# Optimization experiments

Hardware: AMD Instinct MI355X
Metric: run time of the kernel (lower is better)

Reference implementation:

```python
import jax, jax.numpy as jnp
from jax import lax
import numpy as np

B, L, E, H, PRED = 2048, 107, 128, 128, 68
NG, NL, D3 = 3, 3, 384  # 3 stacked GRUs, 3 layers each, padded input dim 3*H


def setup_inputs() -> dict:
    key = jax.random.key(0)
    ks = jax.random.split(key, 10)
    s = 0.08  # ~1/sqrt(H), matches torch GRU init scale
    return {
        "encoded_sequence": jax.random.randint(ks[0], (B, L), 0, 14),
        "encoded_structure": jax.random.randint(ks[1], (B, L), 0, 14),
        "encoded_predicted_loop_type": jax.random.randint(ks[2], (B, L), 0, 14),
        "embed_table": jax.random.normal(ks[3], (14, E), jnp.float32) * s,
        "w_ih": jax.random.normal(ks[4], (NG, NL, 2, 3 * H, D3), jnp.float32) * s,
        "w_hh": jax.random.normal(ks[5], (NG, NL, 2, 3 * H, H), jnp.float32) * s,
        "b_ih": jax.random.normal(ks[6], (NG, NL, 2, 3 * H), jnp.float32) * s,
        "b_hh": jax.random.normal(ks[7], (NG, NL, 2, 3 * H), jnp.float32) * s,
        "lin_w": jax.random.normal(ks[8], (2 * H, 3), jnp.float32) * s,
        "lin_b": jax.random.normal(ks[9], (3,), jnp.float32) * s,
    }


def _gru_dir(x, Wih, Whh, bih, bhh, reverse):
    # x: [B, L, D3]; Wih: [3H, D3]; Whh: [3H, H]. PyTorch gate order: r, z, n.
    xp = jnp.einsum('bld,gd->blg', x, Wih) + bih  # precompute input projections [B,L,3H]
    if reverse:
        xp = xp[:, ::-1]

    def step(h, xt):
        gh = h @ Whh.T + bhh  # [B, 3H]
        xr, xz, xn = jnp.split(xt, 3, axis=-1)
        hr, hz, hn = jnp.split(gh, 3, axis=-1)
        r = jax.nn.sigmoid(xr + hr)
        z = jax.nn.sigmoid(xz + hz)
        n = jnp.tanh(xn + r * hn)
        hnew = (1.0 - z) * n + z * h
        return hnew, hnew

    h0 = jnp.zeros((x.shape[0], H), x.dtype)
    _, hs = lax.scan(step, h0, jnp.swapaxes(xp, 0, 1))  # [L, B, H]
    hs = jnp.swapaxes(hs, 0, 1)
    return hs[:, ::-1] if reverse else hs


def _pad_feat(x):
    d = x.shape[-1]
    return x if d == D3 else jnp.pad(x, ((0, 0), (0, 0), (0, D3 - d)))


def reference(encoded_sequence, encoded_structure, encoded_predicted_loop_type,
              embed_table, w_ih, w_hh, b_ih, b_hh, lin_w, lin_b):
    tok = jnp.stack([encoded_sequence, encoded_structure,
                     encoded_predicted_loop_type], axis=-1)  # [B, L, 3]
    out = embed_table[tok].reshape(tok.shape[0], L, 3 * E)  # [B, L, 384]
    for g in range(NG):
        for l in range(NL):
            xin = _pad_feat(out)
            f = _gru_dir(xin, w_ih[g, l, 0], w_hh[g, l, 0], b_ih[g, l, 0], b_hh[g, l, 0], False)
            b = _gru_dir(xin, w_ih[g, l, 1], w_hh[g, l, 1], b_ih[g, l, 1], b_hh[g, l, 1], True)
            out = jnp.concatenate([f, b], axis=-1)  # [B, L, 2H]
    return out[:, :PRED] @ lin_w + lin_b  # [B, pred_len, 3]
```

## Files before the change

### kernel.cpp

```cpp
#include <hip/hip_runtime.h>
#include <hip/hip_bf16.h>

#define B_ 2048
#define L_ 107
#define E_ 128
#define H_ 128
#define PRED_ 68
#define M_ (B_*L_)

typedef __bf16 bf16;
typedef __bf16 bf16x8 __attribute__((ext_vector_type(8)));
typedef __bf16 bf16x4 __attribute__((ext_vector_type(4)));
typedef float f32x4 __attribute__((ext_vector_type(4)));

__device__ __forceinline__ void gload16(const void* g, void* l) {
  __builtin_amdgcn_global_load_lds(
      (const __attribute__((address_space(1))) unsigned int*)g,
      (__attribute__((address_space(3))) unsigned int*)l, 16, 0, 0);
}

__device__ __forceinline__ float sigm(float x)  { return 1.f / (1.f + __expf(-x)); }
__device__ __forceinline__ float tanhx(float x) { return 1.f - 2.f / (1.f + __expf(2.f * x)); }

__global__ void pack_wih_k(const float* __restrict__ w_ih, bf16* __restrict__ out) {
  int idx = blockIdx.x * 256 + threadIdx.x;
  if (idx >= 9*12*6*8*64*8) return;
  int e = idx & 7;
  int lane = (idx >> 3) & 63;
  int q = idx >> 9;
  int nt = q & 7; q >>= 3;
  int nb = q % 6; q /= 6;
  int kt = q % 12; int gl = q / 12;
  int ng = nb*128 + nt*16 + (lane & 15);
  int k  = kt*32 + (lane >> 4)*8 + e;
  int d  = (ng >= 384) ? 1 : 0;
  int np = ng - d*384;
  float v = w_ih[(((size_t)(gl*2 + d)*384 + np)*384 + k)];
  out[idx] = (bf16)v;
}

__global__ void pack_whh_k(const float* __restrict__ w_hh, bf16* __restrict__ out) {
  int idx = blockIdx.x * 256 + threadIdx.x;
  if (idx >= 9*2*4*24*64*8) return;
  int e = idx & 7;
  int lane = (idx >> 3) & 63;
  int q = idx >> 9;
  int nt = q % 24; q /= 24;
  int ks = q & 3;  q >>= 2;
  int d  = q & 1;  int gl = q >> 1;
  int n = nt*16 + (lane & 15);
  int k = ks*32 + (lane >> 4)*8 + e;
  out[idx] = (bf16)w_hh[((size_t)(gl*2 + d)*384 + n)*128 + k];
}

__global__ void pack_bias_k(const float* __restrict__ b_ih, const float* __restrict__ b_hh,
                            float* __restrict__ bias, float* __restrict__ bhhn) {
  int idx = blockIdx.x * 256 + threadIdx.x;
  if (idx < 9*768) {
    int gl = idx / 768; int n = idx % 768;
    int d = (n >= 384) ? 1 : 0; int np = n - d*384;
    float v = b_ih[(gl*2 + d)*384 + np];
    if (np < 256) v += b_hh[(gl*2 + d)*384 + np];
    bias[idx] = v;
  }
  if (idx < 9*256) {
    int gl = idx / 256; int r = idx % 256;
    int d = (r >= 128) ? 1 : 0; int j = r & 127;
    bhhn[idx] = b_hh[(gl*2 + d)*384 + 256 + j];
  }
}

__global__ void shadow_k(const bf16* __restrict__ X, bf16* __restrict__ shlo,
                         bf16* __restrict__ shhi) {
  int idx = blockIdx.x * 256 + threadIdx.x;
  const int NLO = 2048*54*16;
  if (idx < NLO) {
    int k8 = idx & 15; int q = idx >> 4; int t = q % 54; int b = q / 54;
    *reinterpret_cast<bf16x8*>(shlo + ((size_t)b*54 + t)*128 + k8*8) =
      *reinterpret_cast<const bf16x8*>(X + ((size_t)b*107 + t)*256 + k8*8);
  } else {
    idx -= NLO;
    int k8 = idx & 15; int q = idx >> 4; int t = 54 + q % 53; int b = q / 53;
    if (b < 2048)
      *reinterpret_cast<bf16x8*>(shhi + ((size_t)b*53 + (t-54))*128 + k8*8) =
        *reinterpret_cast<const bf16x8*>(X + ((size_t)b*107 + t)*256 + 128 + k8*8);
  }
}

__global__ __launch_bounds__(256) void gemm_proj_k(
    const bf16* __restrict__ Xin, const bf16* __restrict__ shlo, const bf16* __restrict__ shhi,
    const int* __restrict__ seq, const int* __restrict__ str, const int* __restrict__ lp,
    const float* __restrict__ table, int L0, int KT,
    const bf16* __restrict__ Bp, const float* __restrict__ bias,
    bf16* __restrict__ xpw, int len, int t0f, int t0b) {
  __shared__ __align__(16) bf16 As[2][128*32];
  __shared__ __align__(16) bf16 Bs[2][512*8];
  __shared__ __align__(16) bf16 TBl[14*136];
  __shared__ int tokl[3*128];
  int tid = threadIdx.x; int lane = tid & 63; int w = tid >> 6;
  int l4 = lane & 15, g4 = lane >> 4;
  int wm = w >> 1, wn = w & 1;
  int tw = blockIdx.x >> 4, mtile = blockIdx.x & 15;
  int nb = blockIdx.y, d = blockIdx.z;
  int t = d ? (t0b - tw) : (t0f + tw);

  int c0 = tid, c1 = tid + 256;
  int r0 = c0 >> 2, cc0 = c0 & 3;
  int r1 = c1 >> 2, cc1 = c1 & 3;
  int sw0 = ((cc0 ^ ((r0 >> 1) & 3)) * 8), sw1 = ((cc1 ^ ((r1 >> 1) & 3)) * 8);
  int b0g = mtile*128 + r0, b1g = mtile*128 + r1;
  const bf16* xr0 = Xin + ((size_t)b0g*107 + t)*256;
  const bf16* xr1 = Xin + ((size_t)b1g*107 + t)*256;
  const bf16 *pLo0, *pHi0, *pLo1, *pHi1;
  if (d == 0) {
    pLo0 = xr0; pHi0 = (t < 54) ? xr0 : (shhi + ((size_t)b0g*53 + (t-54))*128 - 128);
    pLo1 = xr1; pHi1 = (t < 54) ? xr1 : (shhi + ((size_t)b1g*53 + (t-54))*128 - 128);
  } else {
    pHi0 = xr0; pLo0 = (t < 54) ? (shlo + ((size_t)b0g*54 + t)*128) : xr0;
    pHi1 = xr1; pLo1 = (t < 54) ? (shlo + ((size_t)b1g*54 + t)*128) : xr1;
  }
  const bf16* Bb = Bp + (size_t)(d*3 + nb) * 4096;

  if (L0) {
    for (int i = tid; i < 1792; i += 256) TBl[(i >> 7)*136 + (i & 127)] = (bf16)table[i];
    if (tid < 128) {
      int b = mtile*128 + tid;
      int g = b*107 + t;
      tokl[tid] = seq[g]; tokl[128 + tid] = str[g]; tokl[256 + tid] = lp[g];
    }
  }

  float bias_r[4];
  #pragma unroll
  for (int nt = 0; nt < 4; ++nt)
    bias_r[nt] = bias[d*384 + nb*128 + wn*64 + nt*16 + l4];

  f32x4 acc[4][4];
  #pragma unroll
  for (int i = 0; i < 4; ++i)
    #pragma unroll
    for (int j = 0; j < 4; ++j) { f32x4 z = {0.f,0.f,0.f,0.f}; acc[i][j] = z; }

  if (!L0) {
    gload16(pLo0 + sw0, &As[0][c0*8]);
    gload16(pLo1 + sw1, &As[0][c1*8]);
  }
  gload16(Bb + c0*8, &Bs[0][c0*8]);
  gload16(Bb + c1*8, &Bs[0][c1*8]);
  __syncthreads();

  for (int kt = 0; kt < KT; ++kt) {
    int cur = kt & 1, nxt = cur ^ 1;
    if (kt + 1 < KT) {
      int k1 = kt + 1;
      if (!L0) {
        gload16((k1 < 4 ? pLo0 : pHi0) + (size_t)k1*32 + sw0, &As[nxt][c0*8]);
        gload16((k1 < 4 ? pLo1 : pHi1) + (size_t)k1*32 + sw1, &As[nxt][c1*8]);
      }
      gload16(Bb + (size_t)k1*6*4096 + c0*8, &Bs[nxt][c0*8]);
      gload16(Bb + (size_t)k1*6*4096 + c1*8, &Bs[nxt][c1*8]);
    }
    bf16x8 af[4], bfr[4];
    if (L0) {
      int ch = kt >> 2; int kc = (kt & 3) * 32;
      #pragma unroll
      for (int mt = 0; mt < 4; ++mt) {
        int r = wm*64 + mt*16 + l4;
        af[mt] = *reinterpret_cast<const bf16x8*>(TBl + tokl[ch*128 + r]*136 + kc + g4*8);
      }
    } else {
      #pragma unroll
      for (int mt = 0; mt < 4; ++mt) {
        int r = wm*64 + mt*16 + l4;
        af[mt] = *reinterpret_cast<const bf16x8*>(&As[cur][r*32 + ((g4 ^ ((r >> 1) & 3)) * 8)]);
      }
    }
    #pragma unroll
    for (int nt = 0; nt < 4; ++nt)
      bfr[nt] = *reinterpret_cast<const bf16x8*>(&Bs[cur][((wn*4 + nt)*64 + lane)*8]);
    #pragma unroll
    for (int mt = 0; mt < 4; ++mt)
      #pragma unroll
      for (int nt = 0; nt < 4; ++nt)
        acc[mt][nt] = __builtin_amdgcn_mfma_f32_16x16x32_bf16(af[mt], bfr[nt], acc[mt][nt], 0, 0, 0);
    __syncthreads();
  }

  int tile_m_base = tw*128 + mtile*8 + wm*4;
  int tile_n_base = nb*8 + wn*4;
  size_t dbase = d ? (size_t)len*128*24*256 : 0;
  #pragma unroll
  for (int mt = 0; mt < 4; ++mt)
    #pragma unroll
    for (int nt = 0; nt < 4; ++nt) {
      f32x4 a = acc[mt][nt]; float bv = bias_r[nt];
      bf16x4 o;
      o[0] = (bf16)(a[0] + bv); o[1] = (bf16)(a[1] + bv);
      o[2] = (bf16)(a[2] + bv); o[3] = (bf16)(a[3] + bv);
      *reinterpret_cast<bf16x4*>(xpw + dbase +
          (((size_t)(tile_m_base + mt)*24 + tile_n_base + nt) << 8) + lane*4) = o;
    }
}

__global__ __launch_bounds__(512, 1) void scan_k(const bf16* __restrict__ xpw,
                                                 const bf16* __restrict__ whh,
                                                 const float* __restrict__ bhhn,
                                                 bf16* __restrict__ xout,
                                                 float* __restrict__ hst,
                                                 int len, int t0f, int t0b, int first) {
  __shared__ __align__(16) bf16 h_lds[2][2048];
  int tid = threadIdx.x; int lane = tid & 63; int w = tid >> 6;
  int l4 = lane & 15, g4 = lane >> 4;
  int d = blockIdx.y;
  int bx = blockIdx.x;
  int b0 = bx * 16;
  const bf16* xpb = xpw + (d ? (size_t)len*128*24*256 : 0);
  int ntl[3] = { w, 8 + w, 16 + w };
  int fragoff = g4*64 + l4*4;
  int j = w*16 + l4;
  int js = j >> 5, jc3 = (j >> 3) & 3, je = j & 7;

  bf16x8 bw[3][4];
  #pragma unroll
  for (int nt = 0; nt < 3; ++nt)
    #pragma unroll
    for (int ks = 0; ks < 4; ++ks)
      bw[nt][ks] = *reinterpret_cast<const bf16x8*>(whh + ((size_t)(d*4 + ks)*24 + ntl[nt])*512 + lane*8);

  float bn = bhhn[d*128 + j];
  float h_own[4];

  if (first) {
    #pragma unroll
    for (int i = 0; i < 4; ++i) h_own[i] = 0.f;
    if (tid < 256) reinterpret_cast<float4*>(&h_lds[0][0])[tid] = make_float4(0.f, 0.f, 0.f, 0.f);
  } else {
    #pragma unroll
    for (int i = 0; i < 4; ++i) {
      h_own[i] = hst[((size_t)d*2048 + b0 + g4*4 + i)*128 + j];
      int m = g4*4 + i;
      h_lds[0][(js*64 + m + 16*jc3)*8 + je] = (bf16)h_own[i];
    }
  }

  bf16x4 xa[3], xb[3];
  {
    #pragma unroll
    for (int nt = 0; nt < 3; ++nt)
      xa[nt] = *reinterpret_cast<const bf16x4*>(xpb + (((size_t)bx*24 + ntl[nt]) << 8) + fragoff);
  }
  __syncthreads();

  auto step = [&](bf16x4 (&xu)[3], bf16x4 (&xl)[3], int tw, int pb) {
    int tc = d ? (t0b - tw) : (t0f + tw);
    int twn = (tw + 1 < len) ? (tw + 1) : (len - 1);
    bf16x8 a[4];
    #pragma unroll
    for (int ks = 0; ks < 4; ++ks)
      a[ks] = *reinterpret_cast<const bf16x8*>(&h_lds[pb][(ks*64 + lane)*8]);
    size_t tmn = (size_t)(twn*128 + bx)*24;
    #pragma unroll
    for (int nt = 0; nt < 3; ++nt)
      xl[nt] = *reinterpret_cast<const bf16x4*>(xpb + ((tmn + ntl[nt]) << 8) + fragoff);
    f32x4 acc[3];
    #pragma unroll
    for (int nt = 0; nt < 3; ++nt) { f32x4 z = {0.f,0.f,0.f,0.f}; acc[nt] = z; }
    #pragma unroll
    for (int ks = 0; ks < 4; ++ks)
      #pragma unroll
      for (int nt = 0; nt < 3; ++nt)
        acc[nt] = __builtin_amdgcn_mfma_f32_16x16x32_bf16(a[ks], bw[nt][ks], acc[nt], 0, 0, 0);
    #pragma unroll
    for (int i = 0; i < 4; ++i) {
      float r = sigm((float)xu[0][i] + acc[0][i]);
      float z = sigm((float)xu[1][i] + acc[1][i]);
      float n = tanhx((float)xu[2][i] + r * (acc[2][i] + bn));
      float hv = (1.f - z) * n + z * h_own[i];
      h_own[i] = hv;
      int m = g4*4 + i;
      h_lds[pb ^ 1][(js*64 + m + 16*jc3)*8 + je] = (bf16)hv;
    }
    __syncthreads();
    if (tid < 256) {
      int mo = tid & 15, sc = tid >> 4;
      int s = sc >> 2, c3 = sc & 3;
      bf16x8 v = *reinterpret_cast<const bf16x8*>(&h_lds[pb ^ 1][s*512 + c3*128 + mo*8]);
      *reinterpret_cast<bf16x8*>(xout + ((size_t)(b0 + mo)*107 + tc)*256 + d*128 + s*32 + c3*8) = v;
    }
  };

  for (int tw = 0; tw < len; ++tw) {
    if (tw & 1) step(xb, xa, tw, 1);
    else        step(xa, xb, tw, 0);
  }
  #pragma unroll
  for (int i = 0; i < 4; ++i)
    hst[((size_t)d*2048 + b0 + g4*4 + i)*128 + j] = h_own[i];
}

__global__ void final_k(const bf16* __restrict__ hs, const float* __restrict__ lw,
                        const float* __restrict__ lb, float* __restrict__ out) {
  __shared__ float wsm[768];
  int tid = threadIdx.x;
  for (int i = tid; i < 768; i += 256) wsm[i] = lw[i];
  __syncthreads();
  int idx = blockIdx.x * 256 + tid;
  int b = idx / 68, t = idx % 68;
  const bf16* row = hs + (size_t)(b*107 + t) * 256;
  float a0 = lb[0], a1 = lb[1], a2 = lb[2];
  for (int j0 = 0; j0 < 256; j0 += 8) {
    bf16x8 v = *reinterpret_cast<const bf16x8*>(row + j0);
    #pragma unroll
    for (int e = 0; e < 8; ++e) {
      float f = (float)v[e];
      a0 += f * wsm[(j0 + e)*3 + 0];
      a1 += f * wsm[(j0 + e)*3 + 1];
      a2 += f * wsm[(j0 + e)*3 + 2];
    }
  }
  out[(size_t)idx*3 + 0] = a0;
  out[(size_t)idx*3 + 1] = a1;
  out[(size_t)idx*3 + 2] = a2;
}

extern "C" void kernel_launch(void* const* d_in, const int* in_sizes, int n_in,
                              void* d_out, int out_size, void* d_ws, size_t ws_size,
                              hipStream_t stream) {
  const int*   seq   = (const int*)d_in[0];
  const int*   str   = (const int*)d_in[1];
  const int*   lp    = (const int*)d_in[2];
  const float* table = (const float*)d_in[3];
  const float* w_ih  = (const float*)d_in[4];
  const float* w_hh  = (const float*)d_in[5];
  const float* b_ih  = (const float*)d_in[6];
  const float* b_hh  = (const float*)d_in[7];
  const float* lw    = (const float*)d_in[8];
  const float* lb    = (const float*)d_in[9];
  float* out = (float*)d_out;
  char* ws = (char*)d_ws;

  const size_t xsz    = (size_t)M_ * 256 * 2;
  const size_t shlosz = (size_t)2048*54*128*2;
  const size_t shhisz = (size_t)2048*53*128*2;
  const size_t wihsz  = (size_t)9*12*6*8*64*8 * 2;
  const size_t whhsz  = (size_t)9*2*4*24*64*8 * 2;
  const size_t biassz = 9*768*4, bhhnsz = 9*256*4;
  const size_t hstsz  = (size_t)2*2048*128*4;
  const size_t fixed  = xsz + shlosz + shhisz + wihsz + whhsz + biassz + bhhnsz + hstsz;
  int W = 32;
  while (W > 8 && fixed + (size_t)2*2048*W*384*2 > ws_size) W -= 8;
  const size_t xpwsz = (size_t)2*2048*W*384*2;

  size_t off = 0;
  bf16* X    = (bf16*)(ws + off); off += xsz;
  bf16* XPW  = (bf16*)(ws + off); off += xpwsz;
  bf16* SHLO = (bf16*)(ws + off); off += shlosz;
  bf16* SHHI = (bf16*)(ws + off); off += shhisz;
  bf16* WIH  = (bf16*)(ws + off); off += wihsz;
  bf16* WHH  = (bf16*)(ws + off); off += whhsz;
  float* BIAS = (float*)(ws + off); off += biassz;
  float* BHHN = (float*)(ws + off); off += bhhnsz;
  float* HST  = (float*)(ws + off);

  hipLaunchKernelGGL(pack_wih_k,  dim3(2654208/256), dim3(256), 0, stream, w_ih, WIH);
  hipLaunchKernelGGL(pack_whh_k,  dim3(884736/256),  dim3(256), 0, stream, w_hh, WHH);
  hipLaunchKernelGGL(pack_bias_k, dim3(27),          dim3(256), 0, stream, b_ih, b_hh, BIAS, BHHN);

  const int phases = (107 + W - 1) / W;
  for (int gl = 0; gl < 9; ++gl) {
    int L0 = (gl == 0) ? 1 : 0;
    int KT = L0 ? 12 : 8;
    if (!L0)
      hipLaunchKernelGGL(shadow_k, dim3(13696), dim3(256), 0, stream, X, SHLO, SHHI);
    for (int p = 0; p < phases; ++p) {
      int len = (107 - p*W < W) ? (107 - p*W) : W;
      int t0f = p*W;
      int t0b = 106 - p*W;
      hipLaunchKernelGGL(gemm_proj_k, dim3(len*16, 3, 2), dim3(256), 0, stream,
                         X, SHLO, SHHI, seq, str, lp, table, L0, KT,
                         WIH + (size_t)gl*294912, BIAS + gl*768, XPW, len, t0f, t0b);
      hipLaunchKernelGGL(scan_k, dim3(128, 2), dim3(512), 0, stream,
                         XPW, WHH + (size_t)gl*98304, BHHN + gl*256, X, HST,
                         len, t0f, t0b, (p == 0) ? 1 : 0);
    }
  }
  hipLaunchKernelGGL(final_k, dim3(544), dim3(256), 0, stream, X, lw, lb, out);
}
```

Before: 3.146 ms.

## Enlarge projection GEMM tile to 256 rows and use explicit vmcnt waits

The input-projection GEMM now covers 256 batch rows per block, with each wave computing a 64x128 output tile, so B-fragment loads are reused across twice as many rows and the grid is halved. The kernel is templated on the embedding-layer flag so the unused paths and shared buffers drop out at compile time. Full __syncthreads are replaced by raw s_barrier plus explicit s_waitcnt vmcnt counts, which lets the next tile's loads stay in flight during the current MFMA work. The cost is a larger accumulator array per thread (more registers, possibly lower occupancy) and fewer blocks per launch.

```diff
diff --git a/kernel.cpp b/kernel.cpp
--- a/kernel.cpp
+++ b/kernel.cpp
@@ -87,112 +87,122 @@
   }
 }
 
+template<int L0>
 __global__ __launch_bounds__(256) void gemm_proj_k(
     const bf16* __restrict__ Xin, const bf16* __restrict__ shlo, const bf16* __restrict__ shhi,
     const int* __restrict__ seq, const int* __restrict__ str, const int* __restrict__ lp,
-    const float* __restrict__ table, int L0, int KT,
+    const float* __restrict__ table, int KT,
     const bf16* __restrict__ Bp, const float* __restrict__ bias,
     bf16* __restrict__ xpw, int len, int t0f, int t0b) {
-  __shared__ __align__(16) bf16 As[2][128*32];
-  __shared__ __align__(16) bf16 Bs[2][512*8];
-  __shared__ __align__(16) bf16 TBl[14*136];
-  __shared__ int tokl[3*128];
+  __shared__ __align__(16) bf16 As[2][256*32];
+  __shared__ __align__(16) bf16 Bs[2][128*32];
+  __shared__ __align__(16) bf16 TBl[L0 ? 14*136 : 1];
+  __shared__ int tokl[L0 ? 3*256 : 1];
   int tid = threadIdx.x; int lane = tid & 63; int w = tid >> 6;
   int l4 = lane & 15, g4 = lane >> 4;
-  int wm = w >> 1, wn = w & 1;
-  int tw = blockIdx.x >> 4, mtile = blockIdx.x & 15;
+  int tw = blockIdx.x >> 3, mtile = blockIdx.x & 7;
   int nb = blockIdx.y, d = blockIdx.z;
   int t = d ? (t0b - tw) : (t0f + tw);
 
+  int rr[4], sw[4];
+  const bf16* pLo[4]; const bf16* pHi[4];
+  #pragma unroll
+  for (int i = 0; i < 4; ++i) {
+    int c = tid + 256*i;
+    int r = c >> 2, cc = c & 3;
+    rr[i] = r; sw[i] = (cc ^ ((r >> 1) & 3)) * 8;
+    int bg = mtile*256 + r;
+    const bf16* xr = Xin + ((size_t)bg*107 + t)*256;
+    if (d == 0) {
+      pLo[i] = xr; pHi[i] = (t < 54) ? xr : (shhi + ((size_t)bg*53 + (t-54))*128 - 128);
+    } else {
+      pHi[i] = xr; pLo[i] = (t < 54) ? (shlo + ((size_t)bg*54 + t)*128) : xr;
+    }
+  }
   int c0 = tid, c1 = tid + 256;
-  int r0 = c0 >> 2, cc0 = c0 & 3;
-  int r1 = c1 >> 2, cc1 = c1 & 3;
-  int sw0 = ((cc0 ^ ((r0 >> 1) & 3)) * 8), sw1 = ((cc1 ^ ((r1 >> 1) & 3)) * 8);
-  int b0g = mtile*128 + r0, b1g = mtile*128 + r1;
-  const bf16* xr0 = Xin + ((size_t)b0g*107 + t)*256;
-  const bf16* xr1 = Xin + ((size_t)b1g*107 + t)*256;
-  const bf16 *pLo0, *pHi0, *pLo1, *pHi1;
-  if (d == 0) {
-    pLo0 = xr0; pHi0 = (t < 54) ? xr0 : (shhi + ((size_t)b0g*53 + (t-54))*128 - 128);
-    pLo1 = xr1; pHi1 = (t < 54) ? xr1 : (shhi + ((size_t)b1g*53 + (t-54))*128 - 128);
-  } else {
-    pHi0 = xr0; pLo0 = (t < 54) ? (shlo + ((size_t)b0g*54 + t)*128) : xr0;
-    pHi1 = xr1; pLo1 = (t < 54) ? (shlo + ((size_t)b1g*54 + t)*128) : xr1;
-  }
   const bf16* Bb = Bp + (size_t)(d*3 + nb) * 4096;
 
-  if (L0) {
+  if constexpr (L0) {
     for (int i = tid; i < 1792; i += 256) TBl[(i >> 7)*136 + (i & 127)] = (bf16)table[i];
-    if (tid < 128) {
-      int b = mtile*128 + tid;
-      int g = b*107 + t;
-      tokl[tid] = seq[g]; tokl[128 + tid] = str[g]; tokl[256 + tid] = lp[g];
-    }
-  }
-
-  float bias_r[4];
-  #pragma unroll
-  for (int nt = 0; nt < 4; ++nt)
-    bias_r[nt] = bias[d*384 + nb*128 + wn*64 + nt*16 + l4];
-
-  f32x4 acc[4][4];
+    for (int i = tid; i < 768; i += 256) {
+      int b = mtile*256 + (i & 255);
+      const int* tokp = (i < 256) ? seq : ((i < 512) ? str : lp);
+      tokl[i] = tokp[b*107 + t];
+    }
+  }
+
+  float bias_r[8];
+  #pragma unroll
+  for (int nt = 0; nt < 8; ++nt)
+    bias_r[nt] = bias[d*384 + nb*128 + nt*16 + l4];
+
+  f32x4 acc[4][8];
   #pragma unroll
   for (int i = 0; i < 4; ++i)
     #pragma unroll
-    for (int j = 0; j < 4; ++j) { f32x4 z = {0.f,0.f,0.f,0.f}; acc[i][j] = z; }
-
-  if (!L0) {
-    gload16(pLo0 + sw0, &As[0][c0*8]);
-    gload16(pLo1 + sw1, &As[0][c1*8]);
+    for (int j = 0; j < 8; ++j) { f32x4 z = {0.f,0.f,0.f,0.f}; acc[i][j] = z; }
+
+  if constexpr (!L0) {
+    #pragma unroll
+    for (int i = 0; i < 4; ++i)
+      gload16(pLo[i] + sw[i], &As[0][(tid + 256*i)*8]);
   }
   gload16(Bb + c0*8, &Bs[0][c0*8]);
   gload16(Bb + c1*8, &Bs[0][c1*8]);
-  __syncthreads();
+  if constexpr (L0) __builtin_amdgcn_s_barrier();
 
   for (int kt = 0; kt < KT; ++kt) {
     int cur = kt & 1, nxt = cur ^ 1;
     if (kt + 1 < KT) {
       int k1 = kt + 1;
-      if (!L0) {
-        gload16((k1 < 4 ? pLo0 : pHi0) + (size_t)k1*32 + sw0, &As[nxt][c0*8]);
-        gload16((k1 < 4 ? pLo1 : pHi1) + (size_t)k1*32 + sw1, &As[nxt][c1*8]);
+      if constexpr (!L0) {
+        #pragma unroll
+        for (int i = 0; i < 4; ++i)
+          gload16((k1 < 4 ? pLo[i] : pHi[i]) + (size_t)k1*32 + sw[i], &As[nxt][(tid + 256*i)*8]);
       }
       gload16(Bb + (size_t)k1*6*4096 + c0*8, &Bs[nxt][c0*8]);
       gload16(Bb + (size_t)k1*6*4096 + c1*8, &Bs[nxt][c1*8]);
-    }
-    bf16x8 af[4], bfr[4];
-    if (L0) {
+      if constexpr (L0) asm volatile("s_waitcnt vmcnt(2)" ::: "memory");
+      else              asm volatile("s_waitcnt vmcnt(6)" ::: "memory");
+    } else {
+      asm volatile("s_waitcnt vmcnt(0)" ::: "memory");
+    }
+    __builtin_amdgcn_s_barrier();
+    __builtin_amdgcn_sched_barrier(0);
+    bf16x8 af[4], bfr[8];
+    if constexpr (L0) {
       int ch = kt >> 2; int kc = (kt & 3) * 32;
       #pragma unroll
       for (int mt = 0; mt < 4; ++mt) {
-        int r = wm*64 + mt*16 + l4;
-        af[mt] = *reinterpret_cast<const bf16x8*>(TBl + tokl[ch*128 + r]*136 + kc + g4*8);
+        int r = w*64 + mt*16 + l4;
+        af[mt] = *reinterpret_cast<const bf16x8*>(TBl + tokl[ch*256 + r]*136 + kc + g4*8);
       }
     } else {
       #pragma unroll
       for (int mt = 0; mt < 4; ++mt) {
-        int r = wm*64 + mt*16 + l4;
+        int r = w*64 + mt*16 + l4;
         af[mt] = *reinterpret_cast<const bf16x8*>(&As[cur][r*32 + ((g4 ^ ((r >> 1) & 3)) * 8)]);
       }
     }
     #pragma unroll
-    for (int nt = 0; nt < 4; ++nt)
-      bfr[nt] = *reinterpret_cast<const bf16x8*>(&Bs[cur][((wn*4 + nt)*64 + lane)*8]);
+    for (int nt = 0; nt < 8; ++nt)
+      bfr[nt] = *reinterpret_cast<const bf16x8*>(&Bs[cur][(nt*64 + lane)*8]);
     #pragma unroll
     for (int mt = 0; mt < 4; ++mt)
       #pragma unroll
-      for (int nt = 0; nt < 4; ++nt)
+      for (int nt = 0; nt < 8; ++nt)
         acc[mt][nt] = __builtin_amdgcn_mfma_f32_16x16x32_bf16(af[mt], bfr[nt], acc[mt][nt], 0, 0, 0);
-    __syncthreads();
-  }
-
-  int tile_m_base = tw*128 + mtile*8 + wm*4;
-  int tile_n_base = nb*8 + wn*4;
+    __builtin_amdgcn_sched_barrier(0);
+    __builtin_amdgcn_s_barrier();
+  }
+
+  int tile_m_base = tw*128 + mtile*16 + w*4;
+  int tile_n_base = nb*8;
   size_t dbase = d ? (size_t)len*128*24*256 : 0;
   #pragma unroll
   for (int mt = 0; mt < 4; ++mt)
     #pragma unroll
-    for (int nt = 0; nt < 4; ++nt) {
+    for (int nt = 0; nt < 8; ++nt) {
       f32x4 a = acc[mt][nt]; float bv = bias_r[nt];
       bf16x4 o;
       o[0] = (bf16)(a[0] + bv); o[1] = (bf16)(a[1] + bv);
@@ -368,17 +378,21 @@
 
   const int phases = (107 + W - 1) / W;
   for (int gl = 0; gl < 9; ++gl) {
-    int L0 = (gl == 0) ? 1 : 0;
-    int KT = L0 ? 12 : 8;
-    if (!L0)
+    int KT = (gl == 0) ? 12 : 8;
+    if (gl != 0)
       hipLaunchKernelGGL(shadow_k, dim3(13696), dim3(256), 0, stream, X, SHLO, SHHI);
     for (int p = 0; p < phases; ++p) {
       int len = (107 - p*W < W) ? (107 - p*W) : W;
       int t0f = p*W;
       int t0b = 106 - p*W;
-      hipLaunchKernelGGL(gemm_proj_k, dim3(len*16, 3, 2), dim3(256), 0, stream,
-                         X, SHLO, SHHI, seq, str, lp, table, L0, KT,
-                         WIH + (size_t)gl*294912, BIAS + gl*768, XPW, len, t0f, t0b);
+      if (gl == 0)
+        hipLaunchKernelGGL(gemm_proj_k<1>, dim3(len*8, 3, 2), dim3(256), 0, stream,
+                           X, SHLO, SHHI, seq, str, lp, table, KT,
+                           WIH + (size_t)gl*294912, BIAS + gl*768, XPW, len, t0f, t0b);
+      else
+        hipLaunchKernelGGL(gemm_proj_k<0>, dim3(len*8, 3, 2), dim3(256), 0, stream,
+                           X, SHLO, SHHI, seq, str, lp, table, KT,
+                           WIH + (size_t)gl*294912, BIAS + gl*768, XPW, len, t0f, t0b);
       hipLaunchKernelGGL(scan_k, dim3(128, 2), dim3(512), 0, stream,
                          XPW, WHH + (size_t)gl*98304, BHHN + gl*256, X, HST,
                          len, t0f, t0b, (p == 0) ? 1 : 0);
```

New measurement: 3.771 ms. 1.2x slower.

## Load GEMM operands directly from global into registers, templatize on first layer

Applied to the files above, without the earlier changes.

The input-projection GEMM no longer stages A and B tiles through LDS with async global-to-LDS loads and per-k barriers. Each wave now loads its own MFMA fragments straight from global memory into registers, with a two-deep software prefetch. The kernel is also templated on the embedding-layer flag so KT and the LDS arrays are compile-time sized. This removes barrier stalls and LDS traffic, at the cost of redundant global loads across waves (A is reread by both N-waves, B by both M-waves) and less coalesced access, relying on the cache.

```diff
diff --git a/kernel.cpp b/kernel.cpp
--- a/kernel.cpp
+++ b/kernel.cpp
@@ -12,12 +12,6 @@
 typedef __bf16 bf16x8 __attribute__((ext_vector_type(8)));
 typedef __bf16 bf16x4 __attribute__((ext_vector_type(4)));
 typedef float f32x4 __attribute__((ext_vector_type(4)));
-
-__device__ __forceinline__ void gload16(const void* g, void* l) {
-  __builtin_amdgcn_global_load_lds(
-      (const __attribute__((address_space(1))) unsigned int*)g,
-      (__attribute__((address_space(3))) unsigned int*)l, 16, 0, 0);
-}
 
 __device__ __forceinline__ float sigm(float x)  { return 1.f / (1.f + __expf(-x)); }
 __device__ __forceinline__ float tanhx(float x) { return 1.f - 2.f / (1.f + __expf(2.f * x)); }
@@ -87,16 +81,16 @@
   }
 }
 
+template<int L0>
 __global__ __launch_bounds__(256) void gemm_proj_k(
     const bf16* __restrict__ Xin, const bf16* __restrict__ shlo, const bf16* __restrict__ shhi,
     const int* __restrict__ seq, const int* __restrict__ str, const int* __restrict__ lp,
-    const float* __restrict__ table, int L0, int KT,
+    const float* __restrict__ table,
     const bf16* __restrict__ Bp, const float* __restrict__ bias,
     bf16* __restrict__ xpw, int len, int t0f, int t0b) {
-  __shared__ __align__(16) bf16 As[2][128*32];
-  __shared__ __align__(16) bf16 Bs[2][512*8];
-  __shared__ __align__(16) bf16 TBl[14*136];
-  __shared__ int tokl[3*128];
+  constexpr int KT = L0 ? 12 : 8;
+  __shared__ __align__(16) bf16 TBl[L0 ? 14*136 : 8];
+  __shared__ int tokl[L0 ? 3*128 : 8];
   int tid = threadIdx.x; int lane = tid & 63; int w = tid >> 6;
   int l4 = lane & 15, g4 = lane >> 4;
   int wm = w >> 1, wn = w & 1;
@@ -104,30 +98,29 @@
   int nb = blockIdx.y, d = blockIdx.z;
   int t = d ? (t0b - tw) : (t0f + tw);
 
-  int c0 = tid, c1 = tid + 256;
-  int r0 = c0 >> 2, cc0 = c0 & 3;
-  int r1 = c1 >> 2, cc1 = c1 & 3;
-  int sw0 = ((cc0 ^ ((r0 >> 1) & 3)) * 8), sw1 = ((cc1 ^ ((r1 >> 1) & 3)) * 8);
-  int b0g = mtile*128 + r0, b1g = mtile*128 + r1;
-  const bf16* xr0 = Xin + ((size_t)b0g*107 + t)*256;
-  const bf16* xr1 = Xin + ((size_t)b1g*107 + t)*256;
-  const bf16 *pLo0, *pHi0, *pLo1, *pHi1;
-  if (d == 0) {
-    pLo0 = xr0; pHi0 = (t < 54) ? xr0 : (shhi + ((size_t)b0g*53 + (t-54))*128 - 128);
-    pLo1 = xr1; pHi1 = (t < 54) ? xr1 : (shhi + ((size_t)b1g*53 + (t-54))*128 - 128);
-  } else {
-    pHi0 = xr0; pLo0 = (t < 54) ? (shlo + ((size_t)b0g*54 + t)*128) : xr0;
-    pHi1 = xr1; pLo1 = (t < 54) ? (shlo + ((size_t)b1g*54 + t)*128) : xr1;
-  }
-  const bf16* Bb = Bp + (size_t)(d*3 + nb) * 4096;
-
-  if (L0) {
+  const bf16* aLo[4]; const bf16* aHi[4];
+  #pragma unroll
+  for (int mt = 0; mt < 4; ++mt) {
+    int b = mtile*128 + wm*64 + mt*16 + l4;
+    const bf16* xr = Xin + ((size_t)b*107 + t)*256;
+    if (d == 0) {
+      aLo[mt] = xr;
+      aHi[mt] = (t < 54) ? xr : (shhi + ((size_t)b*53 + (t-54))*128 - 128);
+    } else {
+      aHi[mt] = xr;
+      aLo[mt] = (t < 54) ? (shlo + ((size_t)b*54 + t)*128) : xr;
+    }
+  }
+  const bf16* Bw = Bp + (size_t)(d*3 + nb)*4096 + (size_t)(wn*4)*512 + lane*8;
+
+  if constexpr (L0) {
     for (int i = tid; i < 1792; i += 256) TBl[(i >> 7)*136 + (i & 127)] = (bf16)table[i];
     if (tid < 128) {
       int b = mtile*128 + tid;
       int g = b*107 + t;
       tokl[tid] = seq[g]; tokl[128 + tid] = str[g]; tokl[256 + tid] = lp[g];
     }
+    __syncthreads();
   }
 
   float bias_r[4];
@@ -141,49 +134,46 @@
     #pragma unroll
     for (int j = 0; j < 4; ++j) { f32x4 z = {0.f,0.f,0.f,0.f}; acc[i][j] = z; }
 
-  if (!L0) {
-    gload16(pLo0 + sw0, &As[0][c0*8]);
-    gload16(pLo1 + sw1, &As[0][c1*8]);
-  }
-  gload16(Bb + c0*8, &Bs[0][c0*8]);
-  gload16(Bb + c1*8, &Bs[0][c1*8]);
-  __syncthreads();
-
-  for (int kt = 0; kt < KT; ++kt) {
-    int cur = kt & 1, nxt = cur ^ 1;
-    if (kt + 1 < KT) {
-      int k1 = kt + 1;
-      if (!L0) {
-        gload16((k1 < 4 ? pLo0 : pHi0) + (size_t)k1*32 + sw0, &As[nxt][c0*8]);
-        gload16((k1 < 4 ? pLo1 : pHi1) + (size_t)k1*32 + sw1, &As[nxt][c1*8]);
+  auto loadA = [&](bf16x8 (&dst)[4], int kt) {
+    if constexpr (L0) {
+      int ch = kt >> 2, kc = (kt & 3) * 32;
+      #pragma unroll
+      for (int mt = 0; mt < 4; ++mt)
+        dst[mt] = *reinterpret_cast<const bf16x8*>(
+            TBl + tokl[ch*128 + wm*64 + mt*16 + l4]*136 + kc + g4*8);
+    } else {
+      if (kt < 4) {
+        #pragma unroll
+        for (int mt = 0; mt < 4; ++mt)
+          dst[mt] = *reinterpret_cast<const bf16x8*>(aLo[mt] + kt*32 + g4*8);
+      } else {
+        #pragma unroll
+        for (int mt = 0; mt < 4; ++mt)
+          dst[mt] = *reinterpret_cast<const bf16x8*>(aHi[mt] + kt*32 + g4*8);
       }
-      gload16(Bb + (size_t)k1*6*4096 + c0*8, &Bs[nxt][c0*8]);
-      gload16(Bb + (size_t)k1*6*4096 + c1*8, &Bs[nxt][c1*8]);
-    }
-    bf16x8 af[4], bfr[4];
-    if (L0) {
-      int ch = kt >> 2; int kc = (kt & 3) * 32;
-      #pragma unroll
-      for (int mt = 0; mt < 4; ++mt) {
-        int r = wm*64 + mt*16 + l4;
-        af[mt] = *reinterpret_cast<const bf16x8*>(TBl + tokl[ch*128 + r]*136 + kc + g4*8);
-      }
-    } else {
-      #pragma unroll
-      for (int mt = 0; mt < 4; ++mt) {
-        int r = wm*64 + mt*16 + l4;
-        af[mt] = *reinterpret_cast<const bf16x8*>(&As[cur][r*32 + ((g4 ^ ((r >> 1) & 3)) * 8)]);
-      }
-    }
+    }
+  };
+  auto loadB = [&](bf16x8 (&dst)[4], int kt) {
     #pragma unroll
     for (int nt = 0; nt < 4; ++nt)
-      bfr[nt] = *reinterpret_cast<const bf16x8*>(&Bs[cur][((wn*4 + nt)*64 + lane)*8]);
+      dst[nt] = *reinterpret_cast<const bf16x8*>(Bw + (size_t)kt*24576 + nt*512);
+  };
+  auto domfma = [&](bf16x8 (&af)[4], bf16x8 (&bfr)[4]) {
     #pragma unroll
     for (int mt = 0; mt < 4; ++mt)
       #pragma unroll
       for (int nt = 0; nt < 4; ++nt)
         acc[mt][nt] = __builtin_amdgcn_mfma_f32_16x16x32_bf16(af[mt], bfr[nt], acc[mt][nt], 0, 0, 0);
-    __syncthreads();
+  };
+
+  bf16x8 af0[4], bf0[4], af1[4], bf1[4];
+  loadA(af0, 0); loadB(bf0, 0);
+  #pragma unroll
+  for (int k2 = 0; k2 < KT; k2 += 2) {
+    if (k2 + 1 < KT) { loadA(af1, k2 + 1); loadB(bf1, k2 + 1); }
+    domfma(af0, bf0);
+    if (k2 + 2 < KT) { loadA(af0, k2 + 2); loadB(bf0, k2 + 2); }
+    if (k2 + 1 < KT) domfma(af1, bf1);
   }
 
   int tile_m_base = tw*128 + mtile*8 + wm*4;
@@ -368,17 +358,20 @@
 
   const int phases = (107 + W - 1) / W;
   for (int gl = 0; gl < 9; ++gl) {
-    int L0 = (gl == 0) ? 1 : 0;
-    int KT = L0 ? 12 : 8;
-    if (!L0)
+    if (gl != 0)
       hipLaunchKernelGGL(shadow_k, dim3(13696), dim3(256), 0, stream, X, SHLO, SHHI);
     for (int p = 0; p < phases; ++p) {
       int len = (107 - p*W < W) ? (107 - p*W) : W;
       int t0f = p*W;
       int t0b = 106 - p*W;
-      hipLaunchKernelGGL(gemm_proj_k, dim3(len*16, 3, 2), dim3(256), 0, stream,
-                         X, SHLO, SHHI, seq, str, lp, table, L0, KT,
-                         WIH + (size_t)gl*294912, BIAS + gl*768, XPW, len, t0f, t0b);
+      if (gl == 0)
+        hipLaunchKernelGGL(gemm_proj_k<1>, dim3(len*16, 3, 2), dim3(256), 0, stream,
+                           X, SHLO, SHHI, seq, str, lp, table,
+                           WIH + (size_t)gl*294912, BIAS + gl*768, XPW, len, t0f, t0b);
+      else
+        hipLaunchKernelGGL(gemm_proj_k<0>, dim3(len*16, 3, 2), dim3(256), 0, stream,
+                           X, SHLO, SHHI, seq, str, lp, table,
+                           WIH + (size_t)gl*294912, BIAS + gl*768, XPW, len, t0f, t0b);
       hipLaunchKernelGGL(scan_k, dim3(128, 2), dim3(512), 0, stream,
                          XPW, WHH + (size_t)gl*98304, BHHN + gl*256, X, HST,
                          len, t0f, t0b, (p == 0) ? 1 : 0);
```

New measurement: 3.554 ms. 13.0% more time.
